# Performance work log

Hardware: AMD Instinct MI355X
Metric: run time of the kernel (lower is better)

## Reference

```python
import jax, jax.numpy as jnp
import numpy as np

BIN_T = 8
BIN1 = 4


def setup_inputs() -> dict:
    key = jax.random.key(0)
    k1, k2, k3, k4 = jax.random.split(key, 4)
    B, input_dim = 4096, 4096
    P = input_dim // BIN_T  # 512 units (k*bin1+j)
    x = jax.random.uniform(k1, (B, input_dim), dtype=jnp.float32)
    # init: (bin_t-1)//4 * rand = 1 * rand for bin_t=8
    t0 = jax.random.uniform(k2, (P,), dtype=jnp.float32)
    t1 = jax.random.uniform(k3, (P,), dtype=jnp.float32)
    t2 = jax.random.uniform(k4, (P,), dtype=jnp.float32)
    return {"x": x, "t0": t0, "t1": t1, "t2": t2}


def _soft_prod(X, axis):
    # torch Product: y = -1 / (-1 + sum(log X))  (reduction over `axis`)
    return -1.0 / (-1.0 + jnp.sum(jnp.log(X), axis=axis))


def reference(x, t0, t1, t2):
    B = x.shape[0]
    P = t0.shape[0]
    # x_part[:, j::bin1] with p = k*bin1 + j  ->  [B, P, bin_t]
    xr = x.reshape(B, -1, BIN_T, BIN1).transpose(0, 1, 3, 2).reshape(B, P, BIN_T)
    l = jnp.arange(BIN_T, dtype=x.dtype)  # also used as m
    # layer-1 interval gates: W1[p, m, l] = sigmoid((l - m) * (m + t2 - l))
    W1 = jax.nn.sigmoid((l[None, None, :] - l[None, :, None])
                        * (l[None, :, None] + t2[:, None, None] - l[None, None, :]))
    # y1[b, p, m] = Product_l(1 - x[b,p,l] * W1[p,m,l]); x_input_layer2 = 1 - y1
    y1 = _soft_prod(1.0 - xr[:, :, None, :] * W1[None], axis=-1)  # [B, P, bin_t]
    # layer-2 gate: W2[p, l]
    W2 = (jax.nn.sigmoid((l[None, :] - t0[:, None]) * (t1[:, None] - l[None, :]))
          * jax.nn.sigmoid((BIN_T - 1 - t2[:, None] - l[None, :]) * l[None, :]))
    # out[b, p] = Product_l(1 - (1 - x_input_layer2) * W2) ; (1 - x_input_layer2) == y1
    out = _soft_prod(1.0 - y1 * W2[None], axis=-1)  # [B, P]
    return out
```

## Files before the change

### kernel.cpp

```cpp
#include <hip/hip_runtime.h>


constexpr int BDIM   = 4096;
constexpr int IN_DIM = 4096;
constexpr int PDIM   = 512;
constexpr int PT = 64;
constexpr int BT = 32;
constexpr float LN2 = 0.69314718055994530942f;

__global__ __launch_bounds__(256, 4)
void box_kernel(const float* __restrict__ x,
                const float* __restrict__ t0,
                const float* __restrict__ t1,
                const float* __restrict__ t2,
                float* __restrict__ out)
{
    __shared__ float w1s[PT][17];
    __shared__ float w2s[PT][9];

    const int p0 = blockIdx.x * PT;
    const int b0 = blockIdx.y * BT;
    const int t  = threadIdx.x;

    if (t < PT) {
        const int p = p0 + t;
        const float t0p = t0[p], t1p = t1[p], t2p = t2[p];
#pragma unroll
        for (int d = -7; d <= 7; ++d) {
            const float fd = (float)d;
            const float z  = fd * (t2p - fd);
            w1s[t][d + 7] = 1.0f / (1.0f + __expf(-z));
        }
#pragma unroll
        for (int m = 0; m < 8; ++m) {
            const float fm = (float)m;
            const float za = (fm - t0p) * (t1p - fm);
            const float zb = (7.0f - t2p - fm) * fm;
            w2s[t][m] = (1.0f / (1.0f + __expf(-za))) * (1.0f / (1.0f + __expf(-zb)));
        }
    }
    __syncthreads();

    const int pl = t & 63;
    const int p  = p0 + pl;
    const int g  = p >> 2;
    const int j  = p & 3;

    float w1d[15];
#pragma unroll
    for (int i = 0; i < 15; ++i) w1d[i] = w1s[pl][i];
    float w2[8];
#pragma unroll
    for (int m = 0; m < 8; ++m) w2[m] = w2s[pl][m];

    const int bstart = b0 + (t >> 6);
    const float* xbase = x + (size_t)bstart * IN_DIM + g * 32 + j;
    float*       obase = out + (size_t)bstart * PDIM + p;

    for (int bi = 0; bi < BT / 4; ++bi) {
        const float* xp = xbase + (size_t)(bi * 4) * IN_DIM;
        float xv[8];
#pragma unroll
        for (int l = 0; l < 8; ++l) xv[l] = xp[l * 4];

        float prod2 = 1.0f;
#pragma unroll
        for (int m = 0; m < 8; ++m) {
            float prod1 = 1.0f;
#pragma unroll
            for (int l = 0; l < 8; ++l)
                prod1 *= (1.0f - xv[l] * w1d[l - m + 7]);
            const float y1 = __builtin_amdgcn_rcpf(1.0f - LN2 * __log2f(prod1));
            prod2 *= (1.0f - y1 * w2[m]);
        }
        obase[(size_t)(bi * 4) * PDIM] =
            __builtin_amdgcn_rcpf(1.0f - LN2 * __log2f(prod2));
    }
}

extern "C" void kernel_launch(void* const* d_in, const int* in_sizes, int n_in,
                              void* d_out, int out_size, void* d_ws, size_t ws_size,
                              hipStream_t stream)
{
    const float* x  = (const float*)d_in[0];
    const float* t0 = (const float*)d_in[1];
    const float* t1 = (const float*)d_in[2];
    const float* t2 = (const float*)d_in[3];
    float* out = (float*)d_out;

    dim3 grid(PDIM / PT, BDIM / BT);
    box_kernel<<<grid, 256, 0, stream>>>(x, t0, t1, t2, out);
}
```

Before: 100.2 us.

## Precompute gate table in separate kernel and stage x via coalesced float4 LDS loads

Moves the sigmoid gate computation into a small pre-kernel that writes a table to workspace, which the main kernel reads directly. Each wave loads x rows with coalesced float4 loads into a double-buffered, XOR-swizzled LDS area and prefetches the next row while computing the current one, replacing the earlier strided scalar global loads. The product reductions become balanced trees, and the batch tile per block is halved. The cost is an extra kernel launch and redundant table reads from global memory in every block.

```diff
diff --git a/kernel.cpp b/kernel.cpp
--- a/kernel.cpp
+++ b/kernel.cpp
@@ -1,80 +1,115 @@
 #include <hip/hip_runtime.h>
 
 
-constexpr int BDIM   = 4096;
 constexpr int IN_DIM = 4096;
 constexpr int PDIM   = 512;
+constexpr int BDIM   = 4096;
 constexpr int PT = 64;
-constexpr int BT = 32;
+constexpr int BT = 16;
 constexpr float LN2 = 0.69314718055994530942f;
 
+__global__ void box_table_kernel(const float* __restrict__ t0,
+                                 const float* __restrict__ t1,
+                                 const float* __restrict__ t2,
+                                 float* __restrict__ tab)
+{
+    const int p = blockIdx.x * blockDim.x + threadIdx.x;
+    if (p >= PDIM) return;
+    const float t0p = t0[p], t1p = t1[p], t2p = t2[p];
+#pragma unroll
+    for (int d = -7; d <= 7; ++d) {
+        const float fd = (float)d;
+        tab[(d + 7) * PDIM + p] = 1.0f / (1.0f + __expf(-(fd * (t2p - fd))));
+    }
+#pragma unroll
+    for (int m = 0; m < 8; ++m) {
+        const float fm = (float)m;
+        const float sa = 1.0f / (1.0f + __expf(-((fm - t0p) * (t1p - fm))));
+        const float sb = 1.0f / (1.0f + __expf(-((7.0f - t2p - fm) * fm)));
+        tab[(15 + m) * PDIM + p] = sa * sb;
+    }
+}
+
 __global__ __launch_bounds__(256, 4)
-void box_kernel(const float* __restrict__ x,
-                const float* __restrict__ t0,
-                const float* __restrict__ t1,
-                const float* __restrict__ t2,
-                float* __restrict__ out)
+void box_main_kernel(const float* __restrict__ x,
+                     const float* __restrict__ tab,
+                     float* __restrict__ out)
 {
-    __shared__ float w1s[PT][17];
-    __shared__ float w2s[PT][9];
+    __shared__ float lds[4][2][512];
 
-    const int p0 = blockIdx.x * PT;
-    const int b0 = blockIdx.y * BT;
-    const int t  = threadIdx.x;
-
-    if (t < PT) {
-        const int p = p0 + t;
-        const float t0p = t0[p], t1p = t1[p], t2p = t2[p];
-#pragma unroll
-        for (int d = -7; d <= 7; ++d) {
-            const float fd = (float)d;
-            const float z  = fd * (t2p - fd);
-            w1s[t][d + 7] = 1.0f / (1.0f + __expf(-z));
-        }
-#pragma unroll
-        for (int m = 0; m < 8; ++m) {
-            const float fm = (float)m;
-            const float za = (fm - t0p) * (t1p - fm);
-            const float zb = (7.0f - t2p - fm) * fm;
-            w2s[t][m] = (1.0f / (1.0f + __expf(-za))) * (1.0f / (1.0f + __expf(-zb)));
-        }
-    }
-    __syncthreads();
-
-    const int pl = t & 63;
-    const int p  = p0 + pl;
-    const int g  = p >> 2;
-    const int j  = p & 3;
+    const int t    = threadIdx.x;
+    const int w    = t >> 6;
+    const int lane = t & 63;
+    const int p0   = blockIdx.x * PT;
+    const int b0   = blockIdx.y * BT;
+    const int p    = p0 + lane;
 
     float w1d[15];
 #pragma unroll
-    for (int i = 0; i < 15; ++i) w1d[i] = w1s[pl][i];
-    float w2[8];
+    for (int i = 0; i < 15; ++i) w1d[i] = tab[i * PDIM + p];
+    float w2v[8];
 #pragma unroll
-    for (int m = 0; m < 8; ++m) w2[m] = w2s[pl][m];
+    for (int m = 0; m < 8; ++m) w2v[m] = tab[(15 + m) * PDIM + p];
 
-    const int bstart = b0 + (t >> 6);
-    const float* xbase = x + (size_t)bstart * IN_DIM + g * 32 + j;
-    float*       obase = out + (size_t)bstart * PDIM + p;
+    const int ls = lane & 7;
+    const int gh = lane >> 3;
+    float* const mybuf  = &lds[w][0][0];
+    float* const wraddr = mybuf + ls * 64 + ((gh ^ ls) << 2);
 
-    for (int bi = 0; bi < BT / 4; ++bi) {
-        const float* xp = xbase + (size_t)(bi * 4) * IN_DIM;
+    const int gr = lane >> 2, jr = lane & 3;
+
+    const int brow = b0 + w * 4;
+    const float* const xrow = x + (size_t)brow * IN_DIM + p0 * 8;
+    float* const orow = out + (size_t)brow * PDIM + p;
+
+    {
+        const float4* s = (const float4*)xrow;
+        float4 a0 = s[lane];
+        float4 a1 = s[64 + lane];
+        *(float4*)(wraddr)      = a0;
+        *(float4*)(wraddr + 32) = a1;
+    }
+
+#pragma unroll
+    for (int r = 0; r < 4; ++r) {
+        float4 n0, n1;
+        if (r < 3) {
+            const float4* s = (const float4*)(xrow + (size_t)(r + 1) * IN_DIM);
+            n0 = s[lane];
+            n1 = s[64 + lane];
+        }
+
+        const float* buf = mybuf + (r & 1) * 512;
         float xv[8];
 #pragma unroll
-        for (int l = 0; l < 8; ++l) xv[l] = xp[l * 4];
+        for (int l = 0; l < 8; ++l)
+            xv[l] = buf[l * 64 + ((gr ^ l) << 2) + jr];
 
-        float prod2 = 1.0f;
+        float c[8];
 #pragma unroll
         for (int m = 0; m < 8; ++m) {
-            float prod1 = 1.0f;
-#pragma unroll
-            for (int l = 0; l < 8; ++l)
-                prod1 *= (1.0f - xv[l] * w1d[l - m + 7]);
-            const float y1 = __builtin_amdgcn_rcpf(1.0f - LN2 * __log2f(prod1));
-            prod2 *= (1.0f - y1 * w2[m]);
+            float f0 = 1.0f - xv[0] * w1d[7 - m];
+            float f1 = 1.0f - xv[1] * w1d[8 - m];
+            float f2 = 1.0f - xv[2] * w1d[9 - m];
+            float f3 = 1.0f - xv[3] * w1d[10 - m];
+            float f4 = 1.0f - xv[4] * w1d[11 - m];
+            float f5 = 1.0f - xv[5] * w1d[12 - m];
+            float f6 = 1.0f - xv[6] * w1d[13 - m];
+            float f7 = 1.0f - xv[7] * w1d[14 - m];
+            const float pr = ((f0 * f1) * (f2 * f3)) * ((f4 * f5) * (f6 * f7));
+            const float y1 = __builtin_amdgcn_rcpf(1.0f - LN2 * __log2f(pr));
+            c[m] = 1.0f - y1 * w2v[m];
         }
-        obase[(size_t)(bi * 4) * PDIM] =
-            __builtin_amdgcn_rcpf(1.0f - LN2 * __log2f(prod2));
+        const float pr2 = ((c[0] * c[1]) * (c[2] * c[3])) * ((c[4] * c[5]) * (c[6] * c[7]));
+        const float res = __builtin_amdgcn_rcpf(1.0f - LN2 * __log2f(pr2));
+
+        if (r < 3) {
+            float* wa = wraddr + (((r + 1) & 1) ? 512 : 0);
+            *(float4*)(wa)      = n0;
+            *(float4*)(wa + 32) = n1;
+        }
+
+        orow[r * PDIM] = res;
     }
 }
 
@@ -87,7 +122,9 @@
     const float* t1 = (const float*)d_in[2];
     const float* t2 = (const float*)d_in[3];
     float* out = (float*)d_out;
+    float* tab = (float*)d_ws;
 
+    box_table_kernel<<<2, 256, 0, stream>>>(t0, t1, t2, tab);
     dim3 grid(PDIM / PT, BDIM / BT);
-    box_kernel<<<grid, 256, 0, stream>>>(x, t0, t1, t2, out);
+    box_main_kernel<<<grid, 256, 0, stream>>>(x, tab, out);
 }
```

Result: no change. 102.2 us (+2.0%).

## Stage x rows through swizzled LDS with float4 loads and algebraic rcp removal

Applied to the files above, without the earlier changes.

Each wave now loads contiguous x rows with coalesced float4 loads into a per-wave double-buffered, XOR-swizzled LDS stage. It prefetches the next two rows while computing the current ones. This replaces the old strided scalar global loads. The inner math is also rewritten so the per-m reciprocal disappears: 1 - y1*w2 is expressed as (den - w2)/den, and the numerator and denominator products are accumulated separately and combined with one log difference. The costs are extra LDS traffic, higher register pressure, and possible overflow or underflow of the accumulated products.

```diff
diff --git a/kernel.cpp b/kernel.cpp
--- a/kernel.cpp
+++ b/kernel.cpp
@@ -1,9 +1,9 @@
 #include <hip/hip_runtime.h>
 
 
-constexpr int BDIM   = 4096;
 constexpr int IN_DIM = 4096;
 constexpr int PDIM   = 512;
+constexpr int BDIM   = 4096;
 constexpr int PT = 64;
 constexpr int BT = 32;
 constexpr float LN2 = 0.69314718055994530942f;
@@ -15,12 +15,14 @@
                 const float* __restrict__ t2,
                 float* __restrict__ out)
 {
-    __shared__ float w1s[PT][17];
-    __shared__ float w2s[PT][9];
+    __shared__ float tabs[PT][25];
+    __shared__ float stage[4][2][2][512];
 
-    const int p0 = blockIdx.x * PT;
-    const int b0 = blockIdx.y * BT;
-    const int t  = threadIdx.x;
+    const int t    = threadIdx.x;
+    const int w    = t >> 6;
+    const int lane = t & 63;
+    const int p0   = blockIdx.x * PT;
+    const int b0   = blockIdx.y * BT;
 
     if (t < PT) {
         const int p = p0 + t;
@@ -28,53 +30,98 @@
 #pragma unroll
         for (int d = -7; d <= 7; ++d) {
             const float fd = (float)d;
-            const float z  = fd * (t2p - fd);
-            w1s[t][d + 7] = 1.0f / (1.0f + __expf(-z));
+            tabs[t][d + 7] = 1.0f / (1.0f + __expf(-(fd * (t2p - fd))));
         }
 #pragma unroll
         for (int m = 0; m < 8; ++m) {
             const float fm = (float)m;
-            const float za = (fm - t0p) * (t1p - fm);
-            const float zb = (7.0f - t2p - fm) * fm;
-            w2s[t][m] = (1.0f / (1.0f + __expf(-za))) * (1.0f / (1.0f + __expf(-zb)));
+            const float sa = 1.0f / (1.0f + __expf(-((fm - t0p) * (t1p - fm))));
+            const float sb = 1.0f / (1.0f + __expf(-((7.0f - t2p - fm) * fm)));
+            tabs[t][15 + m] = sa * sb;
         }
     }
     __syncthreads();
 
-    const int pl = t & 63;
-    const int p  = p0 + pl;
-    const int g  = p >> 2;
-    const int j  = p & 3;
+    float w1d[15], w2v[8];
+#pragma unroll
+    for (int i = 0; i < 15; ++i) w1d[i] = tabs[lane][i];
+#pragma unroll
+    for (int m = 0; m < 8; ++m) w2v[m] = tabs[lane][15 + m];
 
-    float w1d[15];
+    const int ls = lane & 7, gh = lane >> 3;
+    const int woff = ls * 64 + ((gh ^ ls) << 2);
+    float* const wbase = &stage[w][0][0][0];
+
+    const int gr = lane >> 2, jr = lane & 3;
+
+    const int brow = b0 + w * 8;
+    const float* const xrow = x + (size_t)brow * IN_DIM + p0 * 8;
+    float* const orow = out + (size_t)brow * PDIM + p0 + lane;
+
+    {
+        const float4* s0 = (const float4*)xrow;
+        const float4* s1 = (const float4*)(xrow + IN_DIM);
+        float4 a0 = s0[lane], a1 = s0[64 + lane];
+        float4 a2 = s1[lane], a3 = s1[64 + lane];
+        *(float4*)(wbase + woff)            = a0;
+        *(float4*)(wbase + woff + 32)       = a1;
+        *(float4*)(wbase + 512 + woff)      = a2;
+        *(float4*)(wbase + 512 + woff + 32) = a3;
+    }
+
 #pragma unroll
-    for (int i = 0; i < 15; ++i) w1d[i] = w1s[pl][i];
-    float w2[8];
+    for (int rb = 0; rb < 4; ++rb) {
+        float4 n0, n1, n2, n3;
+        if (rb < 3) {
+            const float4* s0 = (const float4*)(xrow + (size_t)(2 * rb + 2) * IN_DIM);
+            const float4* s1 = (const float4*)(xrow + (size_t)(2 * rb + 3) * IN_DIM);
+            n0 = s0[lane]; n1 = s0[64 + lane];
+            n2 = s1[lane]; n3 = s1[64 + lane];
+        }
+
+        const float* buf = wbase + (rb & 1) * 1024;
+        float xr[2][8];
 #pragma unroll
-    for (int m = 0; m < 8; ++m) w2[m] = w2s[pl][m];
+        for (int l = 0; l < 8; ++l) {
+            const int a = l * 64 + ((gr ^ l) << 2) + jr;
+            xr[0][l] = buf[a];
+            xr[1][l] = buf[512 + a];
+        }
 
-    const int bstart = b0 + (t >> 6);
-    const float* xbase = x + (size_t)bstart * IN_DIM + g * 32 + j;
-    float*       obase = out + (size_t)bstart * PDIM + p;
+        float res[2];
+#pragma unroll
+        for (int row = 0; row < 2; ++row) {
+            float Pn = 1.0f, Pd = 1.0f;
+#pragma unroll
+            for (int m = 0; m < 8; ++m) {
+                float f0 = 1.0f - xr[row][0] * w1d[7 - m];
+                float f1 = 1.0f - xr[row][1] * w1d[8 - m];
+                float f2 = 1.0f - xr[row][2] * w1d[9 - m];
+                float f3 = 1.0f - xr[row][3] * w1d[10 - m];
+                float f4 = 1.0f - xr[row][4] * w1d[11 - m];
+                float f5 = 1.0f - xr[row][5] * w1d[12 - m];
+                float f6 = 1.0f - xr[row][6] * w1d[13 - m];
+                float f7 = 1.0f - xr[row][7] * w1d[14 - m];
+                const float p1 = ((f0 * f1) * (f2 * f3)) * ((f4 * f5) * (f6 * f7));
+                const float den = 1.0f - LN2 * __log2f(p1);
+                const float num = den - w2v[m];
+                Pn *= num;
+                Pd *= den;
+            }
+            res[row] = __builtin_amdgcn_rcpf(
+                1.0f - LN2 * (__log2f(Pn) - __log2f(Pd)));
+        }
 
-    for (int bi = 0; bi < BT / 4; ++bi) {
-        const float* xp = xbase + (size_t)(bi * 4) * IN_DIM;
-        float xv[8];
-#pragma unroll
-        for (int l = 0; l < 8; ++l) xv[l] = xp[l * 4];
+        if (rb < 3) {
+            float* wa = wbase + ((rb + 1) & 1) * 1024 + woff;
+            *(float4*)(wa)            = n0;
+            *(float4*)(wa + 32)       = n1;
+            *(float4*)(wa + 512)      = n2;
+            *(float4*)(wa + 512 + 32) = n3;
+        }
 
-        float prod2 = 1.0f;
-#pragma unroll
-        for (int m = 0; m < 8; ++m) {
-            float prod1 = 1.0f;
-#pragma unroll
-            for (int l = 0; l < 8; ++l)
-                prod1 *= (1.0f - xv[l] * w1d[l - m + 7]);
-            const float y1 = __builtin_amdgcn_rcpf(1.0f - LN2 * __log2f(prod1));
-            prod2 *= (1.0f - y1 * w2[m]);
-        }
-        obase[(size_t)(bi * 4) * PDIM] =
-            __builtin_amdgcn_rcpf(1.0f - LN2 * __log2f(prod2));
+        orow[(size_t)(2 * rb) * PDIM]     = res[0];
+        orow[(size_t)(2 * rb + 1) * PDIM] = res[1];
     }
 }
 
```

After: 100.1 us. About the same (-0.2%).
